# Kernel optimization log

Hardware: AMD Instinct MI355X
Metric: run time of the kernel (lower is better)

## Reference

```python
import jax, jax.numpy as jnp
import numpy as np

B, T, C = 2, 2048, 2048
NUM_HEADS, NUM_KV_HEADS, HEAD_DIM = 16, 4, 128
ROPE_THETA = 10000.0
SOFTCAP = 50.0


def sine_table(features, length, min_timescale=1.0, max_timescale=10000.0):
    fraction = jnp.arange(0, features, 2, dtype=jnp.float32) / features
    timescale = min_timescale * (max_timescale / min_timescale) ** fraction
    sinusoid = jnp.arange(length, dtype=jnp.float32)[:, None] / timescale[None, :]
    sinusoid = jnp.concatenate([sinusoid, sinusoid], axis=-1)
    return jnp.sin(sinusoid), jnp.cos(sinusoid)


def rotate_half(x):
    x1, x2 = jnp.split(x, 2, axis=-1)
    return jnp.concatenate([-x2, x1], axis=-1)


def setup_inputs() -> dict:
    key = jax.random.key(0)
    k1, k2, k3, k4, k5 = jax.random.split(key, 5)
    x = jax.random.normal(k1, (B, T, C), dtype=jnp.float32)
    mask = jnp.tril(jnp.ones((T, T), dtype=bool))[None, None]  # causal [1,1,T,T]
    mask = jnp.broadcast_to(mask, (B, 1, T, T))
    std = 0.02
    q_kernel = std * jax.random.normal(k2, (C, NUM_HEADS * HEAD_DIM), dtype=jnp.float32)
    k_kernel = std * jax.random.normal(k3, (C, NUM_KV_HEADS * HEAD_DIM), dtype=jnp.float32)
    v_kernel = std * jax.random.normal(k4, (C, NUM_KV_HEADS * HEAD_DIM), dtype=jnp.float32)
    out_kernel = std * jax.random.normal(k5, (NUM_HEADS * HEAD_DIM, C), dtype=jnp.float32)
    return {"x": x, "mask": mask, "q_kernel": q_kernel, "k_kernel": k_kernel,
            "v_kernel": v_kernel, "out_kernel": out_kernel}


def reference(x, mask, q_kernel, k_kernel, v_kernel, out_kernel):
    _, t, c = x.shape
    r = NUM_HEADS // NUM_KV_HEADS  # GQA group size
    qp = q_kernel.reshape(c, r, NUM_KV_HEADS, HEAD_DIM)
    kp = k_kernel.reshape(c, NUM_KV_HEADS, HEAD_DIM)
    vp = v_kernel.reshape(c, NUM_KV_HEADS, HEAD_DIM)
    op = out_kernel.reshape(r, NUM_KV_HEADS, HEAD_DIM, c)
    q = jnp.einsum('bsm,mrhk->brhsk', x, qp)   # [B,r,h,T,hd]
    k = jnp.einsum('bdm,mhk->bhdk', x, kp)     # [B,h,T,hd]
    v = jnp.einsum('bdm,mhv->bhdv', x, vp)     # [B,h,T,hd]
    sin, cos = sine_table(HEAD_DIM, t, max_timescale=ROPE_THETA)  # [T,hd]
    q = q * cos + rotate_half(q) * sin  # broadcast over leading dims (time at -2)
    k = k * cos + rotate_half(k) * sin
    scale = jax.lax.rsqrt(jnp.array(HEAD_DIM, dtype=x.dtype))
    qk = jnp.einsum('brhsk,bhdk->brhsd', q, k) * scale  # [B,r,h,T,T]
    qk = jnp.tanh(qk / SOFTCAP) * SOFTCAP  # logit softcap
    m = jnp.expand_dims(mask, axis=1)  # [B,1,1,T,T]
    qk = jax.nn.softmax(qk.astype(jnp.float32), where=m).astype(x.dtype)
    qkv = jnp.einsum('brhsd,bhdv->brhsv', qk, v)
    out = jnp.einsum('brhsv,rhvm->bsm', qkv, op)
    return out
```

## Files before the change

### kernel.cpp

```cpp
#include <hip/hip_runtime.h>
#include <hip/hip_bf16.h>

typedef __hip_bfloat16 bf16;
typedef __attribute__((ext_vector_type(8))) short bf16x8;
typedef __attribute__((ext_vector_type(4))) short bf16x4;
typedef __attribute__((ext_vector_type(4))) float f32x4;

#define BATCH 2
#define SEQ 2048
#define CDIM 2048
#define NH 16
#define NKV 4
#define HD 128
#define NQKV 3072
#define GK 2048

__device__ __forceinline__ void gl_lds16(const bf16* g, bf16* l) {
    typedef const __attribute__((address_space(1))) unsigned int* gp_t;
    typedef __attribute__((address_space(3))) unsigned int* lp_t;
    __builtin_amdgcn_global_load_lds((gp_t)g, (lp_t)l, 16, 0, 0);
}

__device__ __forceinline__ f32x4 mfma16x16x16_bf16(bf16x4 a, bf16x4 b, f32x4 c) {
#if __has_builtin(__builtin_amdgcn_mfma_f32_16x16x16bf16_1k)
    return __builtin_amdgcn_mfma_f32_16x16x16bf16_1k(a, b, c, 0, 0, 0);
#else
    asm volatile("v_mfma_f32_16x16x16_bf16 %0, %1, %2, %0"
                 : "+v"(c) : "v"(a), "v"(b));
    return c;
#endif
}

__device__ __forceinline__ float fast_exp2(float x) {
#if __has_builtin(__builtin_amdgcn_exp2f)
    return __builtin_amdgcn_exp2f(x);
#else
    return exp2f(x);
#endif
}

__device__ __forceinline__ float softcap_exp(float u) {
    float t2 = u * u;
    float w = fmaf(t2, -1.328448e-7f, 0.12753101f);
    return fast_exp2(u * w);
}

__global__ __launch_bounds__(256) void f2b_kernel(const float* __restrict__ in,
                                                  bf16* __restrict__ out, int n4)
{
    int i = blockIdx.x * 256 + threadIdx.x;
    if (i >= n4) return;
    float4 v = *(const float4*)&in[(size_t)i * 4];
    bf16 o[4] = {__float2bfloat16(v.x), __float2bfloat16(v.y),
                 __float2bfloat16(v.z), __float2bfloat16(v.w)};
    *(ushort4*)&out[(size_t)i * 4] = *(ushort4*)o;
}

__global__ __launch_bounds__(256) void transpose_f2b_kernel(
    const float* __restrict__ in, bf16* __restrict__ out, int R, int Cn)
{
    __shared__ float tile[64][65];
    const int r0 = blockIdx.y * 64, c0 = blockIdx.x * 64;
    for (int f = threadIdx.x; f < 4096; f += 256) {
        int r = f >> 6, c = f & 63;
        tile[r][c] = in[(size_t)(r0 + r) * Cn + c0 + c];
    }
    __syncthreads();
    for (int f = threadIdx.x; f < 4096; f += 256) {
        int r = f >> 6, c = f & 63;
        out[(size_t)(c0 + r) * R + r0 + c] = __float2bfloat16(tile[c][r]);
    }
}

template <int MODE>
__global__ __launch_bounds__(512, 1) void gemm256_kernel(
    const bf16* __restrict__ A, const bf16* __restrict__ Bt,
    float* __restrict__ C, bf16* __restrict__ Qr, bf16* __restrict__ Kr,
    bf16* __restrict__ Vt)
{
    __shared__ __align__(16) bf16 lds[65536];

    const int tid  = threadIdx.x;
    const int lane = tid & 63;
    const int wid  = tid >> 6;
    const int quad = lane >> 4;
    const int l16  = lane & 15;
    const int m0 = blockIdx.y * 256;
    const int n0 = blockIdx.x * 256;

    const int sr = tid >> 3;
    const int sc = ((tid & 7) ^ (sr & 7)) * 8;
    const bf16* gA = A  + (size_t)(m0 + sr) * GK + sc;
    const bf16* gB = Bt + (size_t)(n0 + sr) * GK + sc;

    int cch[2];
#pragma unroll
    for (int kk = 0; kk < 2; ++kk)
        cch[kk] = (((kk * 4 + quad) ^ (l16 & 7)) << 3);
    int abase[2];
#pragma unroll
    for (int mi = 0; mi < 2; ++mi) {
        int gr = wid * 32 + mi * 16 + l16;
        abase[mi] = ((gr >> 7) << 13) + ((gr & 127) << 6);
    }

    f32x4 acc[2][16];
#pragma unroll
    for (int mi = 0; mi < 2; ++mi)
#pragma unroll
        for (int ni = 0; ni < 16; ++ni)
            acc[mi][ni] = (f32x4){0.f, 0.f, 0.f, 0.f};

#define STAGE_HALF(dstElemBase, srcPtr)                                    \
    {                                                                      \
        bf16* d_ = &lds[(dstElemBase)];                                    \
        gl_lds16((srcPtr),            d_ + tid * 8);                       \
        gl_lds16((srcPtr) + 64 * GK,  d_ + 4096 + tid * 8);                \
    }

    STAGE_HALF(0,         gA);
    STAGE_HALF(8192,      gA + 128 * GK);
    STAGE_HALF(16384,     gB);
    STAGE_HALF(24576,     gB + 128 * GK);
    asm volatile("s_waitcnt vmcnt(0)" ::: "memory");
    __builtin_amdgcn_s_barrier();

    const int NT = GK / 64;
    int p = 0;
    int kt = 0;
    bf16x8 af[2][2], bfr[4][2];

    for (int j = 0; j < NT; ++j) {
        const int ktn = kt + 64;
        const bool pf = (j + 1 < NT);
        const int pw = (p ^ 1) * 32768;
        const int pr = p * 32768;

        if (pf) STAGE_HALF(pw, gA + ktn);
#pragma unroll
        for (int mi = 0; mi < 2; ++mi)
#pragma unroll
            for (int kk = 0; kk < 2; ++kk)
                af[mi][kk] = *(const bf16x8*)&lds[pr + abase[mi] + cch[kk]];
#pragma unroll
        for (int q = 0; q < 4; ++q) {
            int br = q * 16 + l16;
            int bb = 16384 + ((br >> 7) << 13) + ((br & 127) << 6);
#pragma unroll
            for (int kk = 0; kk < 2; ++kk)
                bfr[q][kk] = *(const bf16x8*)&lds[pr + bb + cch[kk]];
        }
        __builtin_amdgcn_s_setprio(1);
#pragma unroll
        for (int q = 0; q < 4; ++q)
#pragma unroll
            for (int mi = 0; mi < 2; ++mi)
#pragma unroll
                for (int kk = 0; kk < 2; ++kk)
                    acc[mi][q] = __builtin_amdgcn_mfma_f32_16x16x32_bf16(
                        af[mi][kk], bfr[q][kk], acc[mi][q], 0, 0, 0);
        __builtin_amdgcn_s_setprio(0);
        asm volatile("" ::: "memory");
        __builtin_amdgcn_s_barrier();

        if (pf) STAGE_HALF(pw + 8192, gA + 128 * GK + ktn);
#pragma unroll
        for (int q = 0; q < 4; ++q) {
            int br = (4 + q) * 16 + l16;
            int bb = 16384 + ((br >> 7) << 13) + ((br & 127) << 6);
#pragma unroll
            for (int kk = 0; kk < 2; ++kk)
                bfr[q][kk] = *(const bf16x8*)&lds[pr + bb + cch[kk]];
        }
        __builtin_amdgcn_s_setprio(1);
#pragma unroll
        for (int q = 0; q < 4; ++q)
#pragma unroll
            for (int mi = 0; mi < 2; ++mi)
#pragma unroll
                for (int kk = 0; kk < 2; ++kk)
                    acc[mi][4 + q] = __builtin_amdgcn_mfma_f32_16x16x32_bf16(
                        af[mi][kk], bfr[q][kk], acc[mi][4 + q], 0, 0, 0);
        __builtin_amdgcn_s_setprio(0);
        asm volatile("s_waitcnt vmcnt(4)" ::: "memory");
        __builtin_amdgcn_s_barrier();

        if (pf) STAGE_HALF(pw + 16384, gB + ktn);
#pragma unroll
        for (int q = 0; q < 4; ++q) {
            int br = (8 + q) * 16 + l16;
            int bb = 16384 + ((br >> 7) << 13) + ((br & 127) << 6);
#pragma unroll
            for (int kk = 0; kk < 2; ++kk)
                bfr[q][kk] = *(const bf16x8*)&lds[pr + bb + cch[kk]];
        }
        __builtin_amdgcn_s_setprio(1);
#pragma unroll
        for (int q = 0; q < 4; ++q)
#pragma unroll
            for (int mi = 0; mi < 2; ++mi)
#pragma unroll
                for (int kk = 0; kk < 2; ++kk)
                    acc[mi][8 + q] = __builtin_amdgcn_mfma_f32_16x16x32_bf16(
                        af[mi][kk], bfr[q][kk], acc[mi][8 + q], 0, 0, 0);
        __builtin_amdgcn_s_setprio(0);
        asm volatile("" ::: "memory");
        __builtin_amdgcn_s_barrier();

        if (pf) STAGE_HALF(pw + 24576, gB + 128 * GK + ktn);
#pragma unroll
        for (int q = 0; q < 4; ++q) {
            int br = (12 + q) * 16 + l16;
            int bb = 16384 + ((br >> 7) << 13) + ((br & 127) << 6);
#pragma unroll
            for (int kk = 0; kk < 2; ++kk)
                bfr[q][kk] = *(const bf16x8*)&lds[pr + bb + cch[kk]];
        }
        __builtin_amdgcn_s_setprio(1);
#pragma unroll
        for (int q = 0; q < 4; ++q)
#pragma unroll
            for (int mi = 0; mi < 2; ++mi)
#pragma unroll
                for (int kk = 0; kk < 2; ++kk)
                    acc[mi][12 + q] = __builtin_amdgcn_mfma_f32_16x16x32_bf16(
                        af[mi][kk], bfr[q][kk], acc[mi][12 + q], 0, 0, 0);
        __builtin_amdgcn_s_setprio(0);
        asm volatile("s_waitcnt vmcnt(2)" ::: "memory");
        __builtin_amdgcn_s_barrier();

        p ^= 1;
        kt = ktn;
    }
#undef STAGE_HALF

    const int mrow0 = m0 + wid * 32;
    if constexpr (MODE == 0) {
#pragma unroll
        for (int mi = 0; mi < 2; ++mi)
#pragma unroll
            for (int ni = 0; ni < 16; ++ni) {
                int col = n0 + ni * 16 + l16;
#pragma unroll
                for (int r = 0; r < 4; ++r) {
                    int row = mrow0 + mi * 16 + quad * 4 + r;
                    C[(size_t)row * CDIM + col] = acc[mi][ni][r];
                }
            }
    } else {
        if (n0 < 2048) {
#pragma unroll
            for (int mi = 0; mi < 2; ++mi)
#pragma unroll
                for (int ni = 0; ni < 16; ++ni) {
                    int col = n0 + ni * 16 + l16;
#pragma unroll
                    for (int r = 0; r < 4; ++r) {
                        int row = mrow0 + mi * 16 + quad * 4 + r;
                        Qr[(size_t)row * 2048 + col] = __float2bfloat16(acc[mi][ni][r]);
                    }
                }
        } else if (n0 < 2560) {
#pragma unroll
            for (int mi = 0; mi < 2; ++mi)
#pragma unroll
                for (int ni = 0; ni < 16; ++ni) {
                    int col = n0 - 2048 + ni * 16 + l16;
#pragma unroll
                    for (int r = 0; r < 4; ++r) {
                        int row = mrow0 + mi * 16 + quad * 4 + r;
                        Kr[(size_t)row * 512 + col] = __float2bfloat16(acc[mi][ni][r]);
                    }
                }
        } else {
#pragma unroll
            for (int mi = 0; mi < 2; ++mi)
#pragma unroll
                for (int ni = 0; ni < 16; ++ni) {
                    int vcol = n0 - 2560 + ni * 16 + l16;
                    int kvh = vcol >> 7, d = vcol & 127;
                    int m = mrow0 + mi * 16 + quad * 4;
                    int bb = m >> 11, t0 = m & 2047;
                    bf16 vb[4];
#pragma unroll
                    for (int r = 0; r < 4; ++r)
                        vb[r] = __float2bfloat16(acc[mi][ni][r]);
                    *(ushort4*)&Vt[((size_t)((bb * NKV + kvh) * HD + d)) * SEQ + t0] =
                        *(ushort4*)vb;
                }
        }
    }
}

__global__ __launch_bounds__(256) void rope_kernel(bf16* __restrict__ data,
                                                   int ncols, int total_pairs)
{
    int idx = blockIdx.x * 256 + threadIdx.x;
    if (idx >= total_pairs) return;
    int half = ncols >> 1;
    int row = idx / half;
    int p = idx - row * half;
    int head = p >> 6;
    int i = p & 63;
    int t = row & (SEQ - 1);
    float inv_ts = expf(-(float)i * 0.14391156831212787f);
    float angle = (float)t * inv_ts;
    float s, c;
    sincosf(angle, &s, &c);
    size_t base = (size_t)row * ncols + head * 128 + i;
    float x1 = __bfloat162float(data[base]);
    float x2 = __bfloat162float(data[base + 64]);
    data[base]      = __float2bfloat16(x1 * c - x2 * s);
    data[base + 64] = __float2bfloat16(x2 * c + x1 * s);
}

template <bool WA>
__device__ __forceinline__ void attn_tile_compute(
    const bf16* __restrict__ Ksr, const bf16* __restrict__ Vtsr,
    const bf16x8 (&qfA)[4], const bf16x8 (&qfB)[4],
    f32x4 (&OA)[8], f32x4 (&OB)[8], float& lsumA, float& lsumB,
    int quad, int l16, int ks, bool diagA, bool diagB, int qselA, int qselB)
{
    f32x4 sA[2], sB[2];
    bf16x4 pfA[2], pfB[2];
#pragma unroll
    for (int mt = 0; mt < 2; ++mt) {
        sB[mt] = (f32x4){0.f, 0.f, 0.f, 0.f};
        if constexpr (WA) sA[mt] = (f32x4){0.f, 0.f, 0.f, 0.f};
        const int krow = (ks * 32 + mt * 16 + l16) * 128;
#pragma unroll
        for (int kk = 0; kk < 4; ++kk) {
            bf16x8 kf = *(const bf16x8*)&Ksr[krow + (((kk * 4 + quad) ^ l16) * 8)];
            sB[mt] = __builtin_amdgcn_mfma_f32_16x16x32_bf16(
                kf, qfB[kk], sB[mt], 0, 0, 0);
            if constexpr (WA)
                sA[mt] = __builtin_amdgcn_mfma_f32_16x16x32_bf16(
                    kf, qfA[kk], sA[mt], 0, 0, 0);
        }
    }
#pragma unroll
    for (int mt = 0; mt < 2; ++mt) {
        bf16 pb[4];
#pragma unroll
        for (int r = 0; r < 4; ++r) {
            float p = softcap_exp(sB[mt][r]);
            if (diagB) {
                int kl = ks * 32 + mt * 16 + quad * 4 + r;
                p = (kl <= qselB) ? p : 0.f;
            }
            lsumB += p;
            pb[r] = __float2bfloat16(p);
        }
        pfB[mt] = *(bf16x4*)pb;
        if constexpr (WA) {
            bf16 pa[4];
#pragma unroll
            for (int r = 0; r < 4; ++r) {
                float p = softcap_exp(sA[mt][r]);
                if (diagA) {
                    int kl = ks * 32 + mt * 16 + quad * 4 + r;
                    p = (kl <= qselA) ? p : 0.f;
                }
                lsumA += p;
                pa[r] = __float2bfloat16(p);
            }
            pfA[mt] = *(bf16x4*)pa;
        }
    }
#pragma unroll
    for (int dj = 0; dj < 8; ++dj) {
        const int vrow = (dj * 16 + l16) * 64;
        const int dl7 = l16 & 7;
#pragma unroll
        for (int mt = 0; mt < 2; ++mt) {
            int c16 = ks * 4 + mt * 2 + (quad >> 1);
            bf16x4 vf = *(const bf16x4*)&Vtsr[vrow + ((c16 ^ dl7) << 3)
                                              + (quad & 1) * 4];
            OB[dj] = mfma16x16x16_bf16(vf, pfB[mt], OB[dj]);
            if constexpr (WA)
                OA[dj] = mfma16x16x16_bf16(vf, pfA[mt], OA[dj]);
        }
    }
}

__global__ __launch_bounds__(512, 2) void attn_mfma12_kernel(
    const bf16* __restrict__ Q, const bf16* __restrict__ K,
    const bf16* __restrict__ Vt, bf16* __restrict__ Att)
{
    __shared__ __align__(16) char smem[70144];

    const int tid = threadIdx.x;
    const int lane = tid & 63;
    const int w = tid >> 6;
    const int ks = w >> 2;
    const int hs = (w >> 1) & 1;
    const int qw = w & 1;
    const int quad = lane >> 4;
    const int l16 = lane & 15;
    const int bh = blockIdx.y;
    const int b   = bh >> 3;
    const int kvh = (bh >> 1) & 3;
    const int pr  = bh & 1;
    const int hq  = kvh + 4 * (pr * 2 + hs);
    const int qlo = blockIdx.x;
    const int qhi = 63 - qlo;
    const int ntlo = (qlo >> 1) + 1;
    const int nthi = (qhi >> 1) + 1;
    const int q0A = qlo * 32 + qw * 16;
    const int q0B = qhi * 32 + qw * 16;

    bf16x8 qfA[4], qfB[4];
    {
        size_t ra = (size_t)(b * SEQ + q0A + l16) * (NH * HD) + hq * HD;
        size_t rb = (size_t)(b * SEQ + q0B + l16) * (NH * HD) + hq * HD;
#pragma unroll
        for (int kk = 0; kk < 4; ++kk) {
            qfA[kk] = *(const bf16x8*)&Q[ra + kk * 32 + quad * 8];
            qfB[kk] = *(const bf16x8*)&Q[rb + kk * 32 + quad * 8];
        }
    }

    f32x4 OA[8], OB[8];
#pragma unroll
    for (int dj = 0; dj < 8; ++dj) {
        OA[dj] = (f32x4){0.f, 0.f, 0.f, 0.f};
        OB[dj] = (f32x4){0.f, 0.f, 0.f, 0.f};
    }
    float lsumA = 0.f, lsumB = 0.f;

    const int qselA = (qlo & 1) * 32 + qw * 16 + l16;
    const int qselB = (qhi & 1) * 32 + qw * 16 + l16;

    const int keyK = tid >> 4;
    const int chK  = (tid & 15) ^ (keyK & 15);
    const int dV   = tid >> 3;
    const int chV  = (tid & 7) ^ (dV & 7);
    const bf16* gK = K  + (size_t)(b * SEQ + keyK) * (NKV * HD) + kvh * HD + chK * 8;
    const bf16* gV = Vt + (size_t)((b * NKV + kvh) * HD + dV) * SEQ + chV * 8;

    {
        bf16* KsW  = (bf16*)smem;
        bf16* VtsW = (bf16*)(smem + 32768);
        gl_lds16(gK,                 KsW + tid * 8);
        gl_lds16(gK + 32 * NKV * HD, KsW + 4096 + tid * 8);
        gl_lds16(gV,                 VtsW + tid * 8);
        gl_lds16(gV + 64 * SEQ,      VtsW + 4096 + tid * 8);
    }
    __syncthreads();

    int cur = 0;
    for (int jt = 0; jt < nthi; ++jt) {
        if (jt + 1 < nthi) {
            gK += 64 * NKV * HD;
            gV += 64;
            bf16* KsW  = (bf16*)(smem + (cur ^ 1) * 16384);
            bf16* VtsW = (bf16*)(smem + 32768 + (cur ^ 1) * 16384);
            gl_lds16(gK,                 KsW + tid * 8);
            gl_lds16(gK + 32 * NKV * HD, KsW + 4096 + tid * 8);
            gl_lds16(gV,                 VtsW + tid * 8);
            gl_lds16(gV + 64 * SEQ,      VtsW + 4096 + tid * 8);
        }
        const bf16* Ksr  = (const bf16*)(smem + cur * 16384);
        const bf16* Vtsr = (const bf16*)(smem + 32768 + cur * 16384);
        const bool diagA = (jt == ntlo - 1);
        const bool diagB = (jt == nthi - 1);
        if (jt < ntlo)
            attn_tile_compute<true>(Ksr, Vtsr, qfA, qfB, OA, OB, lsumA, lsumB,
                                    quad, l16, ks, diagA, diagB, qselA, qselB);
        else
            attn_tile_compute<false>(Ksr, Vtsr, qfA, qfB, OA, OB, lsumA, lsumB,
                                     quad, l16, ks, diagA, diagB, qselA, qselB);
        __syncthreads();
        cur ^= 1;
    }

    float* Osh = (float*)smem;
    float* Lsh = (float*)(smem + 69632);
    const int p = hs * 2 + qw;
    const int ob = (p * 64 + lane) * 68;
    if (ks == 1) {
#pragma unroll
        for (int dj = 0; dj < 8; ++dj) {
            *(f32x4*)&Osh[ob + dj * 4]      = OA[dj];
            *(f32x4*)&Osh[ob + 32 + dj * 4] = OB[dj];
        }
        float vA = lsumA;
        vA += __shfl_xor(vA, 16);
        vA += __shfl_xor(vA, 32);
        float vB = lsumB;
        vB += __shfl_xor(vB, 16);
        vB += __shfl_xor(vB, 32);
        if (quad == 0) {
            Lsh[p * 32 + l16]      = vA;
            Lsh[p * 32 + 16 + l16] = vB;
        }
    }
    __syncthreads();
    if (ks == 0) {
        {
            float v = lsumA;
            v += __shfl_xor(v, 16);
            v += __shfl_xor(v, 32);
            v += Lsh[p * 32 + l16];
            float inv = 1.f / v;
            size_t obase = (size_t)(b * SEQ + q0A + l16) * (NH * HD) + hq * HD;
#pragma unroll
            for (int dj = 0; dj < 8; ++dj) {
                f32x4 o = OA[dj] + *(const f32x4*)&Osh[ob + dj * 4];
                bf16 obuf[4];
#pragma unroll
                for (int r = 0; r < 4; ++r)
                    obuf[r] = __float2bfloat16(o[r] * inv);
                *(ushort4*)&Att[obase + dj * 16 + quad * 4] = *(ushort4*)obuf;
            }
        }
        {
            float v = lsumB;
            v += __shfl_xor(v, 16);
            v += __shfl_xor(v, 32);
            v += Lsh[p * 32 + 16 + l16];
            float inv = 1.f / v;
            size_t obase = (size_t)(b * SEQ + q0B + l16) * (NH * HD) + hq * HD;
#pragma unroll
            for (int dj = 0; dj < 8; ++dj) {
                f32x4 o = OB[dj] + *(const f32x4*)&Osh[ob + 32 + dj * 4];
                bf16 obuf[4];
#pragma unroll
                for (int r = 0; r < 4; ++r)
                    obuf[r] = __float2bfloat16(o[r] * inv);
                *(ushort4*)&Att[obase + dj * 16 + quad * 4] = *(ushort4*)obuf;
            }
        }
    }
}

extern "C" void kernel_launch(void* const* d_in, const int* in_sizes, int n_in,
                              void* d_out, int out_size, void* d_ws, size_t ws_size,
                              hipStream_t stream) {
    const float* x        = (const float*)d_in[0];
    const float* q_kernel = (const float*)d_in[2];
    const float* k_kernel = (const float*)d_in[3];
    const float* v_kernel = (const float*)d_in[4];
    const float* o_kernel = (const float*)d_in[5];
    float* out = (float*)d_out;

    const int M = BATCH * SEQ;
    char* ws = (char*)d_ws;
    bf16* xb   = (bf16*)ws;
    bf16* Att  = xb;
    bf16* wT   = (bf16*)(ws + 16777216);
    bf16* wTq  = wT;
    bf16* wTk  = wT + (size_t)2048 * 2048;
    bf16* wTv  = wT + (size_t)2560 * 2048;
    bf16* woT  = wT;
    bf16* Qr   = (bf16*)(ws + 29360128);
    bf16* Kr   = (bf16*)(ws + 46137344);
    bf16* Vt_g = (bf16*)(ws + 50331648);

    f2b_kernel<<<(M * CDIM / 4 + 255) / 256, 256, 0, stream>>>(x, xb, M * CDIM / 4);
    transpose_f2b_kernel<<<dim3((NH * HD) / 64, CDIM / 64), 256, 0, stream>>>(
        q_kernel, wTq, CDIM, NH * HD);
    transpose_f2b_kernel<<<dim3((NKV * HD) / 64, CDIM / 64), 256, 0, stream>>>(
        k_kernel, wTk, CDIM, NKV * HD);
    transpose_f2b_kernel<<<dim3((NKV * HD) / 64, CDIM / 64), 256, 0, stream>>>(
        v_kernel, wTv, CDIM, NKV * HD);

    gemm256_kernel<1><<<dim3(NQKV / 256, M / 256), 512, 0, stream>>>(
        xb, wT, nullptr, Qr, Kr, Vt_g);

    transpose_f2b_kernel<<<dim3(CDIM / 64, CDIM / 64), 256, 0, stream>>>(
        o_kernel, woT, CDIM, CDIM);

    {
        int pairs_q = M * (NH * HD / 2);
        rope_kernel<<<pairs_q / 256, 256, 0, stream>>>(Qr, NH * HD, pairs_q);
        int pairs_k = M * (NKV * HD / 2);
        rope_kernel<<<pairs_k / 256, 256, 0, stream>>>(Kr, NKV * HD, pairs_k);
    }

    attn_mfma12_kernel<<<dim3(SEQ / 64, BATCH * NKV * 2), 512, 0, stream>>>(
        Qr, Kr, Vt_g, Att);

    gemm256_kernel<0><<<dim3(CDIM / 256, M / 256), 512, 0, stream>>>(
        Att, woT, out, nullptr, nullptr, nullptr);
}
```

Measured before the change: 366.4 us.

## Use 2x4 wave grid with 128x64 warp tiles and whole-tile prefetch

Changes the 256x256 GEMM's wave decomposition from eight 32x256 row strips to a 2x4 grid of 128x64 warp tiles. This raises per-wave operand reuse and cuts LDS reads per MFMA. It also replaces the four-phase staggered staging with a single full-tile prefetch per k-step and one __syncthreads. The trade-off is that the fine-grained interleaving of loads and compute is lost, and the barrier waits for all outstanding loads.

```diff
diff --git a/kernel.cpp b/kernel.cpp
--- a/kernel.cpp
+++ b/kernel.cpp
@@ -83,6 +83,8 @@
     const int tid  = threadIdx.x;
     const int lane = tid & 63;
     const int wid  = tid >> 6;
+    const int wr   = wid >> 2;
+    const int wc   = wid & 3;
     const int quad = lane >> 4;
     const int l16  = lane & 15;
     const int m0 = blockIdx.y * 256;
@@ -97,150 +99,83 @@
 #pragma unroll
     for (int kk = 0; kk < 2; ++kk)
         cch[kk] = (((kk * 4 + quad) ^ (l16 & 7)) << 3);
-    int abase[2];
-#pragma unroll
-    for (int mi = 0; mi < 2; ++mi) {
-        int gr = wid * 32 + mi * 16 + l16;
+    int abase[8];
+#pragma unroll
+    for (int mi = 0; mi < 8; ++mi) {
+        int gr = wr * 128 + mi * 16 + l16;
         abase[mi] = ((gr >> 7) << 13) + ((gr & 127) << 6);
     }
-
-    f32x4 acc[2][16];
-#pragma unroll
-    for (int mi = 0; mi < 2; ++mi)
-#pragma unroll
-        for (int ni = 0; ni < 16; ++ni)
+    int bbase[4];
+#pragma unroll
+    for (int ni = 0; ni < 4; ++ni) {
+        int br = wc * 64 + ni * 16 + l16;
+        bbase[ni] = 16384 + ((br >> 7) << 13) + ((br & 127) << 6);
+    }
+
+    f32x4 acc[8][4];
+#pragma unroll
+    for (int mi = 0; mi < 8; ++mi)
+#pragma unroll
+        for (int ni = 0; ni < 4; ++ni)
             acc[mi][ni] = (f32x4){0.f, 0.f, 0.f, 0.f};
 
-#define STAGE_HALF(dstElemBase, srcPtr)                                    \
+#define STAGE_TILE(bufBase, koff)                                          \
     {                                                                      \
-        bf16* d_ = &lds[(dstElemBase)];                                    \
-        gl_lds16((srcPtr),            d_ + tid * 8);                       \
-        gl_lds16((srcPtr) + 64 * GK,  d_ + 4096 + tid * 8);                \
-    }
-
-    STAGE_HALF(0,         gA);
-    STAGE_HALF(8192,      gA + 128 * GK);
-    STAGE_HALF(16384,     gB);
-    STAGE_HALF(24576,     gB + 128 * GK);
-    asm volatile("s_waitcnt vmcnt(0)" ::: "memory");
-    __builtin_amdgcn_s_barrier();
+        bf16* d_ = &lds[(bufBase)];                                        \
+        gl_lds16(gA + (koff),            d_ + tid * 8);                    \
+        gl_lds16(gA + (koff) + 64 * GK,  d_ + 4096 + tid * 8);             \
+        gl_lds16(gA + (koff) + 128 * GK, d_ + 8192 + tid * 8);             \
+        gl_lds16(gA + (koff) + 192 * GK, d_ + 12288 + tid * 8);            \
+        gl_lds16(gB + (koff),            d_ + 16384 + tid * 8);            \
+        gl_lds16(gB + (koff) + 64 * GK,  d_ + 20480 + tid * 8);            \
+        gl_lds16(gB + (koff) + 128 * GK, d_ + 24576 + tid * 8);            \
+        gl_lds16(gB + (koff) + 192 * GK, d_ + 28672 + tid * 8);            \
+    }
+
+    STAGE_TILE(0, 0);
+    __syncthreads();
 
     const int NT = GK / 64;
     int p = 0;
-    int kt = 0;
-    bf16x8 af[2][2], bfr[4][2];
-
     for (int j = 0; j < NT; ++j) {
-        const int ktn = kt + 64;
-        const bool pf = (j + 1 < NT);
-        const int pw = (p ^ 1) * 32768;
+        if (j + 1 < NT) STAGE_TILE((p ^ 1) * 32768, (j + 1) * 64);
         const int pr = p * 32768;
 
-        if (pf) STAGE_HALF(pw, gA + ktn);
-#pragma unroll
-        for (int mi = 0; mi < 2; ++mi)
+        bf16x8 bfr[4][2];
+#pragma unroll
+        for (int ni = 0; ni < 4; ++ni)
 #pragma unroll
             for (int kk = 0; kk < 2; ++kk)
-                af[mi][kk] = *(const bf16x8*)&lds[pr + abase[mi] + cch[kk]];
-#pragma unroll
-        for (int q = 0; q < 4; ++q) {
-            int br = q * 16 + l16;
-            int bb = 16384 + ((br >> 7) << 13) + ((br & 127) << 6);
+                bfr[ni][kk] = *(const bf16x8*)&lds[pr + bbase[ni] + cch[kk]];
+
+#pragma unroll
+        for (int mi = 0; mi < 8; ++mi) {
+            bf16x8 af[2];
 #pragma unroll
             for (int kk = 0; kk < 2; ++kk)
-                bfr[q][kk] = *(const bf16x8*)&lds[pr + bb + cch[kk]];
-        }
-        __builtin_amdgcn_s_setprio(1);
-#pragma unroll
-        for (int q = 0; q < 4; ++q)
-#pragma unroll
-            for (int mi = 0; mi < 2; ++mi)
+                af[kk] = *(const bf16x8*)&lds[pr + abase[mi] + cch[kk]];
+            __builtin_amdgcn_s_setprio(1);
+#pragma unroll
+            for (int ni = 0; ni < 4; ++ni)
 #pragma unroll
                 for (int kk = 0; kk < 2; ++kk)
-                    acc[mi][q] = __builtin_amdgcn_mfma_f32_16x16x32_bf16(
-                        af[mi][kk], bfr[q][kk], acc[mi][q], 0, 0, 0);
-        __builtin_amdgcn_s_setprio(0);
-        asm volatile("" ::: "memory");
-        __builtin_amdgcn_s_barrier();
-
-        if (pf) STAGE_HALF(pw + 8192, gA + 128 * GK + ktn);
-#pragma unroll
-        for (int q = 0; q < 4; ++q) {
-            int br = (4 + q) * 16 + l16;
-            int bb = 16384 + ((br >> 7) << 13) + ((br & 127) << 6);
-#pragma unroll
-            for (int kk = 0; kk < 2; ++kk)
-                bfr[q][kk] = *(const bf16x8*)&lds[pr + bb + cch[kk]];
-        }
-        __builtin_amdgcn_s_setprio(1);
-#pragma unroll
-        for (int q = 0; q < 4; ++q)
-#pragma unroll
-            for (int mi = 0; mi < 2; ++mi)
-#pragma unroll
-                for (int kk = 0; kk < 2; ++kk)
-                    acc[mi][4 + q] = __builtin_amdgcn_mfma_f32_16x16x32_bf16(
-                        af[mi][kk], bfr[q][kk], acc[mi][4 + q], 0, 0, 0);
-        __builtin_amdgcn_s_setprio(0);
-        asm volatile("s_waitcnt vmcnt(4)" ::: "memory");
-        __builtin_amdgcn_s_barrier();
-
-        if (pf) STAGE_HALF(pw + 16384, gB + ktn);
-#pragma unroll
-        for (int q = 0; q < 4; ++q) {
-            int br = (8 + q) * 16 + l16;
-            int bb = 16384 + ((br >> 7) << 13) + ((br & 127) << 6);
-#pragma unroll
-            for (int kk = 0; kk < 2; ++kk)
-                bfr[q][kk] = *(const bf16x8*)&lds[pr + bb + cch[kk]];
-        }
-        __builtin_amdgcn_s_setprio(1);
-#pragma unroll
-        for (int q = 0; q < 4; ++q)
-#pragma unroll
-            for (int mi = 0; mi < 2; ++mi)
-#pragma unroll
-                for (int kk = 0; kk < 2; ++kk)
-                    acc[mi][8 + q] = __builtin_amdgcn_mfma_f32_16x16x32_bf16(
-                        af[mi][kk], bfr[q][kk], acc[mi][8 + q], 0, 0, 0);
-        __builtin_amdgcn_s_setprio(0);
-        asm volatile("" ::: "memory");
-        __builtin_amdgcn_s_barrier();
-
-        if (pf) STAGE_HALF(pw + 24576, gB + 128 * GK + ktn);
-#pragma unroll
-        for (int q = 0; q < 4; ++q) {
-            int br = (12 + q) * 16 + l16;
-            int bb = 16384 + ((br >> 7) << 13) + ((br & 127) << 6);
-#pragma unroll
-            for (int kk = 0; kk < 2; ++kk)
-                bfr[q][kk] = *(const bf16x8*)&lds[pr + bb + cch[kk]];
-        }
-        __builtin_amdgcn_s_setprio(1);
-#pragma unroll
-        for (int q = 0; q < 4; ++q)
-#pragma unroll
-            for (int mi = 0; mi < 2; ++mi)
-#pragma unroll
-                for (int kk = 0; kk < 2; ++kk)
-                    acc[mi][12 + q] = __builtin_amdgcn_mfma_f32_16x16x32_bf16(
-                        af[mi][kk], bfr[q][kk], acc[mi][12 + q], 0, 0, 0);
-        __builtin_amdgcn_s_setprio(0);
-        asm volatile("s_waitcnt vmcnt(2)" ::: "memory");
-        __builtin_amdgcn_s_barrier();
-
+                    acc[mi][ni] = __builtin_amdgcn_mfma_f32_16x16x32_bf16(
+                        af[kk], bfr[ni][kk], acc[mi][ni], 0, 0, 0);
+            __builtin_amdgcn_s_setprio(0);
+        }
+        __syncthreads();
         p ^= 1;
-        kt = ktn;
-    }
-#undef STAGE_HALF
-
-    const int mrow0 = m0 + wid * 32;
+    }
+#undef STAGE_TILE
+
+    const int mrow0 = m0 + wr * 128;
+    const int ncol0 = n0 + wc * 64;
     if constexpr (MODE == 0) {
 #pragma unroll
-        for (int mi = 0; mi < 2; ++mi)
-#pragma unroll
-            for (int ni = 0; ni < 16; ++ni) {
-                int col = n0 + ni * 16 + l16;
+        for (int mi = 0; mi < 8; ++mi)
+#pragma unroll
+            for (int ni = 0; ni < 4; ++ni) {
+                int col = ncol0 + ni * 16 + l16;
 #pragma unroll
                 for (int r = 0; r < 4; ++r) {
                     int row = mrow0 + mi * 16 + quad * 4 + r;
@@ -250,10 +185,10 @@
     } else {
         if (n0 < 2048) {
 #pragma unroll
-            for (int mi = 0; mi < 2; ++mi)
-#pragma unroll
-                for (int ni = 0; ni < 16; ++ni) {
-                    int col = n0 + ni * 16 + l16;
+            for (int mi = 0; mi < 8; ++mi)
+#pragma unroll
+                for (int ni = 0; ni < 4; ++ni) {
+                    int col = ncol0 + ni * 16 + l16;
 #pragma unroll
                     for (int r = 0; r < 4; ++r) {
                         int row = mrow0 + mi * 16 + quad * 4 + r;
@@ -262,10 +197,10 @@
                 }
         } else if (n0 < 2560) {
 #pragma unroll
-            for (int mi = 0; mi < 2; ++mi)
-#pragma unroll
-                for (int ni = 0; ni < 16; ++ni) {
-                    int col = n0 - 2048 + ni * 16 + l16;
+            for (int mi = 0; mi < 8; ++mi)
+#pragma unroll
+                for (int ni = 0; ni < 4; ++ni) {
+                    int col = ncol0 - 2048 + ni * 16 + l16;
 #pragma unroll
                     for (int r = 0; r < 4; ++r) {
                         int row = mrow0 + mi * 16 + quad * 4 + r;
@@ -274,10 +209,10 @@
                 }
         } else {
 #pragma unroll
-            for (int mi = 0; mi < 2; ++mi)
-#pragma unroll
-                for (int ni = 0; ni < 16; ++ni) {
-                    int vcol = n0 - 2560 + ni * 16 + l16;
+            for (int mi = 0; mi < 8; ++mi)
+#pragma unroll
+                for (int ni = 0; ni < 4; ++ni) {
+                    int vcol = ncol0 - 2560 + ni * 16 + l16;
                     int kvh = vcol >> 7, d = vcol & 127;
                     int m = mrow0 + mi * 16 + quad * 4;
                     int bb = m >> 11, t0 = m & 2047;
```

Measured after the change: 365.9 us. No clear change (-0.1%).
